# Performance work log

Measured on AMD Instinct MI355X. Metric: run time of the kernel, lower is better.

## Reference

```python
import jax, jax.numpy as jnp
import numpy as np

GAMMA = 0.99
B, S, V = 16, 4096, 128
TRUNC = 11  # original code sums over t in range(seqlen - 11)


def setup_inputs() -> dict:
    key = jax.random.key(0)
    k1, k2 = jax.random.split(key)
    log_probs = jax.random.normal(k1, (S, B, V), dtype=jnp.float32)
    logits = jax.random.normal(k2, (B, S, V), dtype=jnp.float32)
    return {"log_probs": log_probs, "logits": logits}


def reference(log_probs, logits):
    # log_probs: [S, B, V] (time-major, as indexed by log_probs[t] in the original)
    # logits:    [B, S, V]
    b, s, v = logits.shape
    # gamma_t starts at gamma for t = S-1 and multiplies each backward step,
    # so r[:, t] gets weight gamma^(S - t) (absolute-position weighting).
    w = jnp.power(jnp.float32(GAMMA), (s - jnp.arange(s)).astype(jnp.float32))  # [S]
    weighted = w[None, :, None] * jax.nn.log_sigmoid(logits)  # [B, S, V]
    # R[t] = sum_{u >= t} weighted[:, u]  -> reverse cumulative sum along seq
    R = jnp.flip(jnp.cumsum(jnp.flip(weighted, axis=1), axis=1), axis=1)  # [B, S, V]
    T = s - TRUNC
    # E_R = sum_{t < T} R[:, t] * log_probs[t]  -> [B, V]
    E_R = jnp.einsum('btv,tbv->bv', R[:, :T], log_probs[:T])
    return E_R
```

## Files before the change

### kernel.cpp

```cpp
#include <hip/hip_runtime.h>

#define B 16
#define S 4096
#define V 128
#define TRUNC 11
#define T_LIM (S - TRUNC)

#define NC 128
#define CT (S / NC)
#define BV (B * V)

#define LOG2_GAMMA (-0.014499569695115089f)
#define INV_GAMMA 1.0101010101010102f

__device__ __forceinline__ float log_sigmoid(float x) {
    float e = __expf(-fabsf(x));
    return fminf(x, 0.0f) - __logf(1.0f + e);
}

__global__ __launch_bounds__(256) void partials_kernel(
    const float4* __restrict__ lp,
    const float4* __restrict__ lg,
    float4* __restrict__ pA,
    float4* __restrict__ pW,
    float4* __restrict__ pL)
{
    int tid = blockIdx.x * blockDim.x + threadIdx.x;
    int v4 = tid & (V / 4 - 1);
    int b  = (tid >> 5) & (B - 1);
    int c  = tid >> 9;
    int t0 = c * CT;

    const float4* lp_p = lp + (size_t)t0 * (B * V / 4) + b * (V / 4) + v4;
    const float4* lg_p = lg + (size_t)b * (S * V / 4) + (size_t)t0 * (V / 4) + v4;

    float w = exp2f(LOG2_GAMMA * (float)(S - t0));

    float ax = 0.f, ay = 0.f, az = 0.f, aw = 0.f;
    float Ax = 0.f, Ay = 0.f, Az = 0.f, Aw = 0.f;
    float Wx = 0.f, Wy = 0.f, Wz = 0.f, Ww = 0.f;

    #pragma unroll 8
    for (int i = 0; i < CT; ++i) {
        int t = t0 + i;
        float4 l = lp_p[(size_t)i * (B * V / 4)];
        float4 x = lg_p[(size_t)i * (V / 4)];
        if (t < T_LIM) {
            ax += l.x; ay += l.y; az += l.z; aw += l.w;
        }
        float sx = w * log_sigmoid(x.x);
        float sy = w * log_sigmoid(x.y);
        float sz = w * log_sigmoid(x.z);
        float sw = w * log_sigmoid(x.w);
        Ax = fmaf(sx, ax, Ax);
        Ay = fmaf(sy, ay, Ay);
        Az = fmaf(sz, az, Az);
        Aw = fmaf(sw, aw, Aw);
        Wx += sx; Wy += sy; Wz += sz; Ww += sw;
        w *= INV_GAMMA;
    }

    pA[tid] = make_float4(Ax, Ay, Az, Aw);
    pW[tid] = make_float4(Wx, Wy, Wz, Ww);
    pL[tid] = make_float4(ax, ay, az, aw);
}

__global__ __launch_bounds__(256) void combine_kernel(
    const float* __restrict__ pA,
    const float* __restrict__ pW,
    const float* __restrict__ pL,
    float* __restrict__ out)
{
    int gtid = blockIdx.x * blockDim.x + threadIdx.x;
    int bv   = gtid >> 6;
    int lane = threadIdx.x & 63;
    if (bv >= BV) return;

    size_t i0 = (size_t)(lane * 2) * BV + bv;
    float A0 = pA[i0], A1 = pA[i0 + BV];
    float W0 = pW[i0], W1 = pW[i0 + BV];
    float L0 = pL[i0], L1 = pL[i0 + BV];

    float s = L0 + L1;

    float scan = s;
    #pragma unroll
    for (int off = 1; off < 64; off <<= 1) {
        float n = __shfl_up(scan, off, 64);
        if (lane >= off) scan += n;
    }
    float base = scan - s;

    float E = A0 + A1;
    E = fmaf(base,      W0, E);
    E = fmaf(base + L0, W1, E);

    #pragma unroll
    for (int off = 32; off > 0; off >>= 1)
        E += __shfl_down(E, off, 64);

    if (lane == 0) out[bv] = E;
}

__global__ __launch_bounds__(256) void direct_kernel(
    const float4* __restrict__ lp,
    const float4* __restrict__ lg,
    float4* __restrict__ out)
{
    int tid = blockIdx.x * blockDim.x + threadIdx.x;
    if (tid >= B * V / 4) return;
    int v4 = tid & (V / 4 - 1);
    int b  = tid >> 5;

    const float4* lp_p = lp + b * (V / 4) + v4;
    const float4* lg_p = lg + (size_t)b * (S * V / 4) + v4;

    float w = exp2f(LOG2_GAMMA * (float)S);
    float ax = 0.f, ay = 0.f, az = 0.f, aw = 0.f;
    float Ax = 0.f, Ay = 0.f, Az = 0.f, Aw = 0.f;
    for (int t = 0; t < S; ++t) {
        float4 l = lp_p[(size_t)t * (B * V / 4)];
        float4 x = lg_p[(size_t)t * (V / 4)];
        if (t < T_LIM) { ax += l.x; ay += l.y; az += l.z; aw += l.w; }
        Ax = fmaf(w * log_sigmoid(x.x), ax, Ax);
        Ay = fmaf(w * log_sigmoid(x.y), ay, Ay);
        Az = fmaf(w * log_sigmoid(x.z), az, Az);
        Aw = fmaf(w * log_sigmoid(x.w), aw, Aw);
        w *= INV_GAMMA;
    }
    out[tid] = make_float4(Ax, Ay, Az, Aw);
}

extern "C" void kernel_launch(void* const* d_in, const int* in_sizes, int n_in,
                              void* d_out, int out_size, void* d_ws, size_t ws_size,
                              hipStream_t stream)
{
    const float4* lp = (const float4*)d_in[0];
    const float4* lg = (const float4*)d_in[1];
    float* out = (float*)d_out;

    size_t per = (size_t)NC * BV;

    if (per * 3 * sizeof(float) > ws_size) {
        direct_kernel<<<(B * V / 4 + 255) / 256, 256, 0, stream>>>(
            lp, lg, (float4*)d_out);
        return;
    }

    float* pA = (float*)d_ws;
    float* pW = pA + per;
    float* pL = pW + per;

    int threads1 = NC * (B * V / 4);
    partials_kernel<<<threads1 / 256, 256, 0, stream>>>(
        lp, lg, (float4*)pA, (float4*)pW, (float4*)pL);

    int threads2 = BV * 64;
    combine_kernel<<<threads2 / 256, 256, 0, stream>>>(pA, pW, pL, out);
}
```

Baseline: 113.6 us.

## Split sequence into more chunks and transpose partials for vectorized combine

Raises the number of sequence chunks from 128 to 512, so the partials kernel launches four times as many threads, each handling a shorter chunk with its loop fully unrolled and the truncation branch replaced by a mask multiply. Partials are now written in a bv-major transposed layout so the combine kernel can read contiguous float4 rows and scan 256 chunks per (b,v) using two interleaved wave scans. The aim is more parallelism and latency hiding in the bandwidth-bound first pass. The cost is a larger workspace, scattered strided scalar stores in the first kernel, and more partial-sum traffic.

```diff
diff --git a/kernel.cpp b/kernel.cpp
--- a/kernel.cpp
+++ b/kernel.cpp
@@ -6,7 +6,7 @@
 #define TRUNC 11
 #define T_LIM (S - TRUNC)
 
-#define NC 128
+#define NC 512
 #define CT (S / NC)
 #define BV (B * V)
 
@@ -21,9 +21,9 @@
 __global__ __launch_bounds__(256) void partials_kernel(
     const float4* __restrict__ lp,
     const float4* __restrict__ lg,
-    float4* __restrict__ pA,
-    float4* __restrict__ pW,
-    float4* __restrict__ pL)
+    float* __restrict__ pA,
+    float* __restrict__ pW,
+    float* __restrict__ pL)
 {
     int tid = blockIdx.x * blockDim.x + threadIdx.x;
     int v4 = tid & (V / 4 - 1);
@@ -40,14 +40,15 @@
     float Ax = 0.f, Ay = 0.f, Az = 0.f, Aw = 0.f;
     float Wx = 0.f, Wy = 0.f, Wz = 0.f, Ww = 0.f;
 
-    #pragma unroll 8
+    #pragma unroll
     for (int i = 0; i < CT; ++i) {
-        int t = t0 + i;
         float4 l = lp_p[(size_t)i * (B * V / 4)];
         float4 x = lg_p[(size_t)i * (V / 4)];
-        if (t < T_LIM) {
-            ax += l.x; ay += l.y; az += l.z; aw += l.w;
-        }
+        float m = (t0 + i < T_LIM) ? 1.0f : 0.0f;
+        ax = fmaf(m, l.x, ax);
+        ay = fmaf(m, l.y, ay);
+        az = fmaf(m, l.z, az);
+        aw = fmaf(m, l.w, aw);
         float sx = w * log_sigmoid(x.x);
         float sy = w * log_sigmoid(x.y);
         float sz = w * log_sigmoid(x.z);
@@ -60,15 +61,19 @@
         w *= INV_GAMMA;
     }
 
-    pA[tid] = make_float4(Ax, Ay, Az, Aw);
-    pW[tid] = make_float4(Wx, Wy, Wz, Ww);
-    pL[tid] = make_float4(ax, ay, az, aw);
+    size_t base = (size_t)(b * V + v4 * 4) * NC + c;
+    pA[base]          = Ax; pA[base + NC]     = Ay;
+    pA[base + 2 * NC] = Az; pA[base + 3 * NC] = Aw;
+    pW[base]          = Wx; pW[base + NC]     = Wy;
+    pW[base + 2 * NC] = Wz; pW[base + 3 * NC] = Ww;
+    pL[base]          = ax; pL[base + NC]     = ay;
+    pL[base + 2 * NC] = az; pL[base + 3 * NC] = aw;
 }
 
 __global__ __launch_bounds__(256) void combine_kernel(
-    const float* __restrict__ pA,
-    const float* __restrict__ pW,
-    const float* __restrict__ pL,
+    const float4* __restrict__ pA,
+    const float4* __restrict__ pW,
+    const float4* __restrict__ pL,
     float* __restrict__ out)
 {
     int gtid = blockIdx.x * blockDim.x + threadIdx.x;
@@ -76,24 +81,38 @@
     int lane = threadIdx.x & 63;
     if (bv >= BV) return;
 
-    size_t i0 = (size_t)(lane * 2) * BV + bv;
-    float A0 = pA[i0], A1 = pA[i0 + BV];
-    float W0 = pW[i0], W1 = pW[i0 + BV];
-    float L0 = pL[i0], L1 = pL[i0 + BV];
+    const int nc4 = NC / 4;
+    const float4* rA = pA + (size_t)bv * nc4;
+    const float4* rW = pW + (size_t)bv * nc4;
+    const float4* rL = pL + (size_t)bv * nc4;
 
-    float s = L0 + L1;
+    float4 A0 = rA[lane], A1 = rA[64 + lane];
+    float4 W0 = rW[lane], W1 = rW[64 + lane];
+    float4 L0 = rL[lane], L1 = rL[64 + lane];
 
-    float scan = s;
+    float a1 = L0.x, a2 = a1 + L0.y, a3 = a2 + L0.z, s0 = a3 + L0.w;
+    float b1 = L1.x, b2 = b1 + L1.y, b3 = b2 + L1.z, s1 = b3 + L1.w;
+
+    float sc0 = s0, sc1 = s1;
     #pragma unroll
     for (int off = 1; off < 64; off <<= 1) {
-        float n = __shfl_up(scan, off, 64);
-        if (lane >= off) scan += n;
+        float n0 = __shfl_up(sc0, off, 64);
+        float n1 = __shfl_up(sc1, off, 64);
+        if (lane >= off) { sc0 += n0; sc1 += n1; }
     }
-    float base = scan - s;
+    float tot0  = __shfl(sc0, 63, 64);
+    float base0 = sc0 - s0;
+    float base1 = tot0 + sc1 - s1;
 
-    float E = A0 + A1;
-    E = fmaf(base,      W0, E);
-    E = fmaf(base + L0, W1, E);
+    float E = A0.x + A0.y + A0.z + A0.w + A1.x + A1.y + A1.z + A1.w;
+    E = fmaf(base0,      W0.x, E);
+    E = fmaf(base0 + a1, W0.y, E);
+    E = fmaf(base0 + a2, W0.z, E);
+    E = fmaf(base0 + a3, W0.w, E);
+    E = fmaf(base1,      W1.x, E);
+    E = fmaf(base1 + b1, W1.y, E);
+    E = fmaf(base1 + b2, W1.z, E);
+    E = fmaf(base1 + b3, W1.w, E);
 
     #pragma unroll
     for (int off = 32; off > 0; off >>= 1)
@@ -152,9 +171,9 @@
     float* pL = pW + per;
 
     int threads1 = NC * (B * V / 4);
-    partials_kernel<<<threads1 / 256, 256, 0, stream>>>(
-        lp, lg, (float4*)pA, (float4*)pW, (float4*)pL);
+    partials_kernel<<<threads1 / 256, 256, 0, stream>>>(lp, lg, pA, pW, pL);
 
     int threads2 = BV * 64;
-    combine_kernel<<<threads2 / 256, 256, 0, stream>>>(pA, pW, pL, out);
+    combine_kernel<<<threads2 / 256, 256, 0, stream>>>(
+        (const float4*)pA, (const float4*)pW, (const float4*)pL, out);
 }
```

After: 121.1 us. 1.07x slower.

## Split sequence into more chunks, preload chunk into registers, widen combine

Applied to the files above, without the earlier changes.

Raises the number of sequence chunks from 128 to 512 so the partials kernel launches four times as many threads, each handling 8 timesteps. Each thread issues all of its loads up front into register arrays, so the memory requests are in flight together, and the truncation branch becomes a multiply by a mask. The combine kernel now has each lane scan 8 chunks serially before the wave-wide scan. In exchange, the workspace of partial results grows fourfold, which adds write and read traffic between the two kernels.

```diff
diff --git a/kernel.cpp b/kernel.cpp
--- a/kernel.cpp
+++ b/kernel.cpp
@@ -6,9 +6,10 @@
 #define TRUNC 11
 #define T_LIM (S - TRUNC)
 
-#define NC 128
+#define NC 512
 #define CT (S / NC)
 #define BV (B * V)
+#define BVq (B * V / 4)
 
 #define LOG2_GAMMA (-0.014499569695115089f)
 #define INV_GAMMA 1.0101010101010102f
@@ -18,7 +19,7 @@
     return fminf(x, 0.0f) - __logf(1.0f + e);
 }
 
-__global__ __launch_bounds__(256) void partials_kernel(
+__global__ __launch_bounds__(256, 4) void partials_kernel(
     const float4* __restrict__ lp,
     const float4* __restrict__ lg,
     float4* __restrict__ pA,
@@ -31,8 +32,14 @@
     int c  = tid >> 9;
     int t0 = c * CT;
 
-    const float4* lp_p = lp + (size_t)t0 * (B * V / 4) + b * (V / 4) + v4;
+    const float4* lp_p = lp + (size_t)t0 * BVq + b * (V / 4) + v4;
     const float4* lg_p = lg + (size_t)b * (S * V / 4) + (size_t)t0 * (V / 4) + v4;
+
+    float4 Lb[CT], Xb[CT];
+    #pragma unroll
+    for (int i = 0; i < CT; ++i) Lb[i] = lp_p[(size_t)i * BVq];
+    #pragma unroll
+    for (int i = 0; i < CT; ++i) Xb[i] = lg_p[(size_t)i * (V / 4)];
 
     float w = exp2f(LOG2_GAMMA * (float)(S - t0));
 
@@ -40,18 +47,17 @@
     float Ax = 0.f, Ay = 0.f, Az = 0.f, Aw = 0.f;
     float Wx = 0.f, Wy = 0.f, Wz = 0.f, Ww = 0.f;
 
-    #pragma unroll 8
+    #pragma unroll
     for (int i = 0; i < CT; ++i) {
-        int t = t0 + i;
-        float4 l = lp_p[(size_t)i * (B * V / 4)];
-        float4 x = lg_p[(size_t)i * (V / 4)];
-        if (t < T_LIM) {
-            ax += l.x; ay += l.y; az += l.z; aw += l.w;
-        }
-        float sx = w * log_sigmoid(x.x);
-        float sy = w * log_sigmoid(x.y);
-        float sz = w * log_sigmoid(x.z);
-        float sw = w * log_sigmoid(x.w);
+        float m = (t0 + i < T_LIM) ? 1.0f : 0.0f;
+        ax = fmaf(m, Lb[i].x, ax);
+        ay = fmaf(m, Lb[i].y, ay);
+        az = fmaf(m, Lb[i].z, az);
+        aw = fmaf(m, Lb[i].w, aw);
+        float sx = w * log_sigmoid(Xb[i].x);
+        float sy = w * log_sigmoid(Xb[i].y);
+        float sz = w * log_sigmoid(Xb[i].z);
+        float sw = w * log_sigmoid(Xb[i].w);
         Ax = fmaf(sx, ax, Ax);
         Ay = fmaf(sy, ay, Ay);
         Az = fmaf(sz, az, Az);
@@ -76,12 +82,23 @@
     int lane = threadIdx.x & 63;
     if (bv >= BV) return;
 
-    size_t i0 = (size_t)(lane * 2) * BV + bv;
-    float A0 = pA[i0], A1 = pA[i0 + BV];
-    float W0 = pW[i0], W1 = pW[i0 + BV];
-    float L0 = pL[i0], L1 = pL[i0 + BV];
+    int c0 = lane * 8;
+    size_t base = (size_t)c0 * BV + bv;
 
-    float s = L0 + L1;
+    float Aj[8], Wj[8], Lj[8];
+    #pragma unroll
+    for (int j = 0; j < 8; ++j) {
+        size_t idx = base + (size_t)j * BV;
+        Aj[j] = pA[idx];
+        Wj[j] = pW[idx];
+        Lj[j] = pL[idx];
+    }
+
+    float p[8];
+    float run = 0.f;
+    #pragma unroll
+    for (int j = 0; j < 8; ++j) { p[j] = run; run += Lj[j]; }
+    float s = run;
 
     float scan = s;
     #pragma unroll
@@ -89,11 +106,12 @@
         float n = __shfl_up(scan, off, 64);
         if (lane >= off) scan += n;
     }
-    float base = scan - s;
+    float lbase = scan - s;
 
-    float E = A0 + A1;
-    E = fmaf(base,      W0, E);
-    E = fmaf(base + L0, W1, E);
+    float E = 0.f;
+    #pragma unroll
+    for (int j = 0; j < 8; ++j)
+        E = fmaf(lbase + p[j], Wj[j], E + Aj[j]);
 
     #pragma unroll
     for (int off = 32; off > 0; off >>= 1)
@@ -119,7 +137,7 @@
     float ax = 0.f, ay = 0.f, az = 0.f, aw = 0.f;
     float Ax = 0.f, Ay = 0.f, Az = 0.f, Aw = 0.f;
     for (int t = 0; t < S; ++t) {
-        float4 l = lp_p[(size_t)t * (B * V / 4)];
+        float4 l = lp_p[(size_t)t * BVq];
         float4 x = lg_p[(size_t)t * (V / 4)];
         if (t < T_LIM) { ax += l.x; ay += l.y; az += l.z; aw += l.w; }
         Ax = fmaf(w * log_sigmoid(x.x), ax, Ax);
```

Measured after the change: 115.7 us. Within noise of the previous version (+1.8%).
